# Kernel optimization log

Measured on AMD Instinct MI355X. Metric: run time of the kernel, lower is better.

The kernel has to match this reference:

```python
import jax, jax.numpy as jnp
import numpy as np

N = 2_097_152
EPS = 1e-6


def _tri(x):
    # triangleWave (period 2), maps R -> [0, 1]; applied to 'normalize=True' tables
    return 2.0 * jnp.abs(x / 2.0 - jnp.floor(x / 2.0 + 0.5))


def _grid2d(uv, table, bilinear, normalize):
    # uv: (N,2) in [0,1); table: (U,V,L)
    t = _tri(table) if normalize else table
    U, V, _ = t.shape
    u = jnp.clip(uv[:, 0], 0.0, 1.0 - EPS) * (U - 1)
    v = jnp.clip(uv[:, 1], 0.0, 1.0 - EPS) * (V - 1)
    if bilinear:
        u0 = jnp.floor(u)
        v0 = jnp.floor(v)
        fu = (u - u0)[:, None]
        fv = (v - v0)[:, None]
        u0i = u0.astype(jnp.int32)
        v0i = v0.astype(jnp.int32)
        u1i = jnp.minimum(u0i + 1, U - 1)
        v1i = jnp.minimum(v0i + 1, V - 1)
        return (t[u0i, v0i] * (1 - fu) * (1 - fv)
                + t[u1i, v0i] * fu * (1 - fv)
                + t[u0i, v1i] * (1 - fu) * fv
                + t[u1i, v1i] * fu * fv)
    return t[jnp.round(u).astype(jnp.int32), jnp.round(v).astype(jnp.int32)]


def _grid1d(u, table, bilinear, normalize):
    # u: (N,) in [0,1); table: (U,L)
    t = _tri(table) if normalize else table
    U, _ = t.shape
    uu = jnp.clip(u, 0.0, 1.0 - EPS) * (U - 1)
    if bilinear:
        u0 = jnp.floor(uu)
        fu = (uu - u0)[:, None]
        u0i = u0.astype(jnp.int32)
        u1i = jnp.minimum(u0i + 1, U - 1)
        return t[u0i] * (1 - fu) + t[u1i] * fu
    return t[jnp.round(uu).astype(jnp.int32)]


def setup_inputs() -> dict:
    key = jax.random.key(0)
    ks = jax.random.split(key, 17)
    mk = lambda i, shape: jax.random.uniform(ks[i], shape, dtype=jnp.float32)
    names = ["roughNoh", "anisoToh", "nDotLV", "tDotLV", "metalLoh",
             "subCg", "spst", "shst", "lumCs"]
    d = {n: mk(i, (N, 2)) for i, n in enumerate(names)}
    d["tabRAEnc"] = mk(9, (2048, 2048, 2))
    d["tabCgEnc"] = mk(10, (2048, 1))
    d["tabRSEnc"] = mk(11, (64, 64, 3))
    d["tabRADec"] = mk(12, (48, 48, 3))
    d["tabCgDec"] = mk(13, (96, 2))
    d["tabLVR"] = mk(14, (32, 32, 1))
    d["tabLV"] = mk(15, (32, 32, 4))
    d["tabNHL"] = mk(16, (32, 32, 4))
    return d


def reference(roughNoh, anisoToh, nDotLV, tDotLV, metalLoh, subCg, spst, shst,
              lumCs, tabRAEnc, tabCgEnc, tabRSEnc, tabRADec, tabCgDec,
              tabLVR, tabLV, tabNHL):
    raIn = jnp.stack((roughNoh[:, 0], anisoToh[:, 0]), axis=1)  # (N,2)
    metallicity = metalLoh[:, 0]
    # ---- encoder: LUT lookups + elementwise mixing coefficients ----
    ra = _grid2d(raIn, tabRAEnc, bilinear=False, normalize=True)           # (N,2)
    cg = _grid1d(subCg[:, 1], tabCgEnc, bilinear=False, normalize=True)    # (N,1)
    rsEnc = _grid2d(jnp.concatenate((raIn[:, 0:1], subCg[:, 0:1]), axis=1),
                    tabRSEnc, bilinear=True, normalize=True)               # (N,3)
    cd = (1 - metallicity) * lumCs[:, 0]
    cm0 = (spst[:, 0] * 0.1 * (1 - metallicity) * spst[:, 1]
           + metallicity * lumCs[:, 0])[:, None]
    cm1 = (spst[:, 0] * 0.1 * (1 - metallicity) * (1 - spst[:, 1]))[:, None]
    cs0 = (shst[:, 0] * (1 - metallicity) * shst[:, 1])[:, None]
    cs1 = (shst[:, 0] * (1 - metallicity) * (1 - shst[:, 1]))[:, None]
    cc = (0.25 * 0.25 * lumCs[:, 1])[:, None]
    rsCd = rsEnc * cd[:, None]                                             # (N,3)
    # ---- decoder LUTs ----
    raCoefs = _grid2d(ra, tabRADec, bilinear=True, normalize=False)        # (N,3)
    cgCoefs = _grid1d(cg[:, 0], tabCgDec, bilinear=True, normalize=False)  # (N,2)
    vTerm = _grid2d(jnp.concatenate((nDotLV[:, 0:1] * nDotLV[:, 1:2],
                                     ra[:, 0:1]), axis=1),
                    tabLVR, bilinear=True, normalize=True)                 # (N,1)
    nlvCoefs = _grid2d(nDotLV, tabLV, bilinear=True, normalize=True)       # (N,4)
    nhlCoefs = _grid2d(jnp.stack((metalLoh[:, 1], nDotLV[:, 0]), axis=1),
                       tabNHL, bilinear=True, normalize=True)              # (N,4)
    # ---- elementwise shading combination ----
    noh2 = roughNoh[:, 1] ** 2
    den = raCoefs[:, 0] * anisoToh[:, 1] ** 2 + raCoefs[:, 1] * noh2 + raCoefs[:, 2]
    dTerm = (0.25 / (nDotLV[:, 1] * den ** 2))[:, None]
    x = (rsCd[:, 0:1] * metalLoh[:, 1:2] * nlvCoefs[:, 1:2]
         + rsCd[:, 1:2] * nlvCoefs[:, 2:3]
         + rsCd[:, 2:3] * nlvCoefs[:, 3:4]
         + cm0 * vTerm * nhlCoefs[:, 2:3] * dTerm
         + cs0 * nhlCoefs[:, 0:1])
    y = (((1 - cm1) * nhlCoefs[:, 3:4] + cm1) * vTerm * dTerm
         + cs1 * nhlCoefs[:, 0:1]
         + cc * nhlCoefs[:, 1:2] * nlvCoefs[:, 0:1]
           / (nDotLV[:, 1] * (cgCoefs[:, 0] * noh2 + cgCoefs[:, 1]))[:, None])
    return jnp.concatenate((x, y), axis=1)  # (N,2)
```

## Files before the change

### kernel.cpp

```cpp
#include <hip/hip_runtime.h>
#include <hip/hip_fp16.h>

#define CLIP_HI (1.0f - 1e-6f)

typedef float f4v __attribute__((ext_vector_type(4)));

__device__ __forceinline__ float tri_(float x) {
    return 2.0f * fabsf(x * 0.5f - floorf(x * 0.5f + 0.5f));
}

__device__ __forceinline__ float clamp01(float x) {
    return fminf(fmaxf(x, 0.0f), CLIP_HI);
}

__device__ __forceinline__ float4 nt_load4(const float* p) {
    f4v v = __builtin_nontemporal_load((const f4v*)p);
    return make_float4(v.x, v.y, v.z, v.w);
}
__device__ __forceinline__ void nt_store4(float* p, float4 v) {
    f4v t = {v.x, v.y, v.z, v.w};
    __builtin_nontemporal_store(t, (f4v*)p);
}

struct H4 { __half2 xy, zw; };

struct BW {
    int i00, i10, i01, i11;
    float w00, w10, w01, w11;
};

template <int U, int V>
__device__ __forceinline__ BW bw2d(float uc, float vc) {
    float u = clamp01(uc) * (float)(U - 1);
    float v = clamp01(vc) * (float)(V - 1);
    float u0f = floorf(u), v0f = floorf(v);
    float fu = u - u0f, fv = v - v0f;
    int u0 = (int)u0f, v0 = (int)v0f;
    BW r;
    r.i00 = u0 * V + v0;
    r.i10 = r.i00 + V;
    r.i01 = r.i00 + 1;
    r.i11 = r.i10 + 1;
    float gu = 1.0f - fu, gv = 1.0f - fv;
    r.w00 = gu * gv; r.w10 = fu * gv; r.w01 = gu * fv; r.w11 = fu * fv;
    return r;
}

__device__ __forceinline__ float4 h4_blend(H4 A, H4 B, H4 C, H4 D, const BW& b) {
    float2 Axy = __half22float2(A.xy), Azw = __half22float2(A.zw);
    float2 Bxy = __half22float2(B.xy), Bzw = __half22float2(B.zw);
    float2 Cxy = __half22float2(C.xy), Czw = __half22float2(C.zw);
    float2 Dxy = __half22float2(D.xy), Dzw = __half22float2(D.zw);
    return make_float4(
        Axy.x * b.w00 + Bxy.x * b.w10 + Cxy.x * b.w01 + Dxy.x * b.w11,
        Axy.y * b.w00 + Bxy.y * b.w10 + Cxy.y * b.w01 + Dxy.y * b.w11,
        Azw.x * b.w00 + Bzw.x * b.w10 + Czw.x * b.w01 + Dzw.x * b.w11,
        Azw.y * b.w00 + Bzw.y * b.w10 + Czw.y * b.w01 + Dzw.y * b.w11);
}

__global__ __launch_bounds__(256) void prep_kernel(const float* __restrict__ t_rs,
                                                   const float* __restrict__ t_cge,
                                                   const float* __restrict__ t_cgd,
                                                   const float* __restrict__ t_rad,
                                                   H4* __restrict__ o_rs,
                                                   __half2* __restrict__ o_cg,
                                                   H4* __restrict__ o_rad) {
    int j = blockIdx.x * 256 + threadIdx.x;
    if (j < 64 * 64) {
        float a = tri_(t_rs[j * 3 + 0]);
        float b = tri_(t_rs[j * 3 + 1]);
        float c = tri_(t_rs[j * 3 + 2]);
        H4 h;
        h.xy = __floats2half2_rn(a, b);
        h.zw = __floats2half2_rn(c, 0.0f);
        o_rs[j] = h;
    }
    if (j < 2048) {
        float cg = tri_(t_cge[j]);
        float u = clamp01(cg) * 95.0f;
        float u0f = floorf(u);
        float fu = u - u0f;
        int u0 = (int)u0f;
        int u1 = min(u0 + 1, 95);
        float2 a = ((const float2*)t_cgd)[u0];
        float2 b = ((const float2*)t_cgd)[u1];
        o_cg[j] = __floats2half2_rn(a.x * (1.0f - fu) + b.x * fu,
                                    a.y * (1.0f - fu) + b.y * fu);
    }
    if (j < 48 * 48) {
        H4 h;
        h.xy = __floats2half2_rn(t_rad[j * 3 + 0], t_rad[j * 3 + 1]);
        h.zw = __floats2half2_rn(t_rad[j * 3 + 2], 0.0f);
        o_rad[j] = h;
    }
}

__device__ __forceinline__ float2 gatherRA(const float* __restrict__ tabRAEnc,
                                           float rNx, float aTx) {
    int ui = (int)rintf(clamp01(rNx) * 2047.0f);
    int vi = (int)rintf(clamp01(aTx) * 2047.0f);
    return ((const float2*)tabRAEnc)[ui * 2048 + vi];
}

template <bool USE_WS>
__device__ __forceinline__ float2 shadeB(
    float rNx, float rNy, float aTy, float nLVx, float nLVy,
    float mLx, float mLy, float sCx, float sCy, float spx, float spy,
    float shx, float shy, float lCx, float lCy,
    float2 raT,
    const float* __restrict__ tabRSEnc, const H4* __restrict__ rsPacked,
    const float* __restrict__ tabRADec, const H4* __restrict__ raDec,
    const float* __restrict__ tabCgEnc, const float* __restrict__ tabCgDec,
    const __half2* __restrict__ cgComp,
    const __half* sLVR, const H4* sLV, const H4* sNHL)
{
    float rs0, rs1, rs2;
    {
        BW b = bw2d<64, 64>(rNx, sCx);
        if constexpr (USE_WS) {
            float4 r = h4_blend(rsPacked[b.i00], rsPacked[b.i10],
                                rsPacked[b.i01], rsPacked[b.i11], b);
            rs0 = r.x; rs1 = r.y; rs2 = r.z;
        } else {
            const float* p00 = tabRSEnc + b.i00 * 3;
            const float* p10 = tabRSEnc + b.i10 * 3;
            const float* p01 = tabRSEnc + b.i01 * 3;
            const float* p11 = tabRSEnc + b.i11 * 3;
            rs0 = tri_(p00[0]) * b.w00 + tri_(p10[0]) * b.w10 + tri_(p01[0]) * b.w01 + tri_(p11[0]) * b.w11;
            rs1 = tri_(p00[1]) * b.w00 + tri_(p10[1]) * b.w10 + tri_(p01[1]) * b.w01 + tri_(p11[1]) * b.w11;
            rs2 = tri_(p00[2]) * b.w00 + tri_(p10[2]) * b.w10 + tri_(p01[2]) * b.w01 + tri_(p11[2]) * b.w11;
        }
    }

    float2 cgC;
    {
        int ci = (int)rintf(clamp01(sCy) * 2047.0f);
        if constexpr (USE_WS) {
            cgC = __half22float2(cgComp[ci]);
        } else {
            float cg = tri_(tabCgEnc[ci]);
            float u = clamp01(cg) * 95.0f;
            float u0f = floorf(u);
            float fu = u - u0f;
            int u0 = (int)u0f;
            int u1 = min(u0 + 1, 95);
            float2 a = ((const float2*)tabCgDec)[u0];
            float2 b = ((const float2*)tabCgDec)[u1];
            cgC = make_float2(a.x * (1.0f - fu) + b.x * fu,
                              a.y * (1.0f - fu) + b.y * fu);
        }
    }

    float4 nlv, nhl;
    {
        BW b = bw2d<32, 32>(nLVx, nLVy);
        nlv = h4_blend(sLV[b.i00], sLV[b.i10], sLV[b.i01], sLV[b.i11], b);
    }
    {
        BW b = bw2d<32, 32>(mLy, nLVx);
        nhl = h4_blend(sNHL[b.i00], sNHL[b.i10], sNHL[b.i01], sNHL[b.i11], b);
    }

    float ra0 = tri_(raT.x);
    float ra1 = tri_(raT.y);

    float raC0, raC1, raC2;
    {
        BW b = bw2d<48, 48>(ra0, ra1);
        if constexpr (USE_WS) {
            float4 r = h4_blend(raDec[b.i00], raDec[b.i10],
                                raDec[b.i01], raDec[b.i11], b);
            raC0 = r.x; raC1 = r.y; raC2 = r.z;
        } else {
            const float* p00 = tabRADec + b.i00 * 3;
            const float* p10 = tabRADec + b.i10 * 3;
            const float* p01 = tabRADec + b.i01 * 3;
            const float* p11 = tabRADec + b.i11 * 3;
            raC0 = p00[0] * b.w00 + p10[0] * b.w10 + p01[0] * b.w01 + p11[0] * b.w11;
            raC1 = p00[1] * b.w00 + p10[1] * b.w10 + p01[1] * b.w01 + p11[1] * b.w11;
            raC2 = p00[2] * b.w00 + p10[2] * b.w10 + p01[2] * b.w01 + p11[2] * b.w11;
        }
    }

    float vTerm;
    {
        BW b = bw2d<32, 32>(nLVx * nLVy, ra0);
        vTerm = __half2float(sLVR[b.i00]) * b.w00 + __half2float(sLVR[b.i10]) * b.w10 +
                __half2float(sLVR[b.i01]) * b.w01 + __half2float(sLVR[b.i11]) * b.w11;
    }

    float met = mLx;
    float om  = 1.0f - met;
    float cd  = om * lCx;
    float cm0 = spx * 0.1f * om * spy + met * lCx;
    float cm1 = spx * 0.1f * om * (1.0f - spy);
    float cs0 = shx * om * shy;
    float cs1 = shx * om * (1.0f - shy);
    float cc  = 0.0625f * lCy;

    float noh2 = rNy * rNy;
    float den  = raC0 * aTy * aTy + raC1 * noh2 + raC2;
    float dTerm = 0.25f / (nLVy * den * den);

    float x = rs0 * cd * mLy * nlv.y + rs1 * cd * nlv.z + rs2 * cd * nlv.w
            + cm0 * vTerm * nhl.z * dTerm + cs0 * nhl.x;

    float y = ((1.0f - cm1) * nhl.w + cm1) * vTerm * dTerm
            + cs1 * nhl.x
            + cc * nhl.y * nlv.x / (nLVy * (cgC.x * noh2 + cgC.y));

    return make_float2(x, y);
}

template <bool USE_WS>
__global__ __launch_bounds__(256, 4) void disney_main(
    const float* __restrict__ roughNoh,
    const float* __restrict__ anisoToh,
    const float* __restrict__ nDotLV,
    const float* __restrict__ metalLoh,
    const float* __restrict__ subCg,
    const float* __restrict__ spst,
    const float* __restrict__ shst,
    const float* __restrict__ lumCs,
    const float* __restrict__ tabRAEnc,
    const float* __restrict__ tabCgEnc,
    const float* __restrict__ tabCgDec,
    const float* __restrict__ tabRSEnc,
    const float* __restrict__ tabRADec,
    const H4*    __restrict__ rsPacked,
    const __half2* __restrict__ cgComp,
    const H4*    __restrict__ raDec,
    const float* __restrict__ tabLVR,
    const float* __restrict__ tabLV,
    const float* __restrict__ tabNHL,
    float* __restrict__ out,
    int n)
{
    __shared__ __half  sLVR[1024];
    __shared__ H4      sLV[1024];
    __shared__ H4      sNHL[1024];

    int tid = threadIdx.x;

#pragma unroll
    for (int k = 0; k < 4; ++k) {
        int j = tid + k * 256;
        sLVR[j] = __float2half(tri_(tabLVR[j]));
        float4 v = ((const float4*)tabLV)[j];
        H4 h; h.xy = __floats2half2_rn(tri_(v.x), tri_(v.y));
              h.zw = __floats2half2_rn(tri_(v.z), tri_(v.w));
        sLV[j] = h;
        float4 w = ((const float4*)tabNHL)[j];
        H4 h2; h2.xy = __floats2half2_rn(tri_(w.x), tri_(w.y));
               h2.zw = __floats2half2_rn(tri_(w.z), tri_(w.w));
        sNHL[j] = h2;
    }
    __syncthreads();

    int P = (n + 1) >> 1;
    int H = (P + 1) >> 1;
    int t = blockIdx.x * 256 + tid;
    if (t >= H) return;
    int p1 = t;
    int p2 = t + H;

    bool full1 = (2 * p1 + 1) < n;
    bool full2 = (p2 < P) && ((2 * p2 + 1) < n);

    if (full1 && full2) {
        float4 rN1 = nt_load4(roughNoh + 4 * p1);
        float4 aT1 = nt_load4(anisoToh + 4 * p1);
        float4 rN2 = nt_load4(roughNoh + 4 * p2);
        float4 aT2 = nt_load4(anisoToh + 4 * p2);

        float2 raT0 = gatherRA(tabRAEnc, rN1.x, aT1.x);
        float2 raT1 = gatherRA(tabRAEnc, rN1.z, aT1.z);
        float2 raT2 = gatherRA(tabRAEnc, rN2.x, aT2.x);
        float2 raT3 = gatherRA(tabRAEnc, rN2.z, aT2.z);

        float4 nLV1 = nt_load4(nDotLV   + 4 * p1);
        float4 mL1  = nt_load4(metalLoh + 4 * p1);
        float4 sC1  = nt_load4(subCg    + 4 * p1);
        float4 sp1  = nt_load4(spst     + 4 * p1);
        float4 sh1  = nt_load4(shst     + 4 * p1);
        float4 lC1  = nt_load4(lumCs    + 4 * p1);
        float4 nLV2 = nt_load4(nDotLV   + 4 * p2);
        float4 mL2  = nt_load4(metalLoh + 4 * p2);
        float4 sC2  = nt_load4(subCg    + 4 * p2);
        float4 sp2  = nt_load4(spst     + 4 * p2);
        float4 sh2  = nt_load4(shst     + 4 * p2);
        float4 lC2  = nt_load4(lumCs    + 4 * p2);

        float2 r0 = shadeB<USE_WS>(rN1.x, rN1.y, aT1.y, nLV1.x, nLV1.y,
                                   mL1.x, mL1.y, sC1.x, sC1.y, sp1.x, sp1.y,
                                   sh1.x, sh1.y, lC1.x, lC1.y, raT0,
                                   tabRSEnc, rsPacked, tabRADec, raDec,
                                   tabCgEnc, tabCgDec, cgComp,
                                   sLVR, sLV, sNHL);
        float2 r1 = shadeB<USE_WS>(rN1.z, rN1.w, aT1.w, nLV1.z, nLV1.w,
                                   mL1.z, mL1.w, sC1.z, sC1.w, sp1.z, sp1.w,
                                   sh1.z, sh1.w, lC1.z, lC1.w, raT1,
                                   tabRSEnc, rsPacked, tabRADec, raDec,
                                   tabCgEnc, tabCgDec, cgComp,
                                   sLVR, sLV, sNHL);
        nt_store4(out + 4 * p1, make_float4(r0.x, r0.y, r1.x, r1.y));

        float2 r2 = shadeB<USE_WS>(rN2.x, rN2.y, aT2.y, nLV2.x, nLV2.y,
                                   mL2.x, mL2.y, sC2.x, sC2.y, sp2.x, sp2.y,
                                   sh2.x, sh2.y, lC2.x, lC2.y, raT2,
                                   tabRSEnc, rsPacked, tabRADec, raDec,
                                   tabCgEnc, tabCgDec, cgComp,
                                   sLVR, sLV, sNHL);
        float2 r3 = shadeB<USE_WS>(rN2.z, rN2.w, aT2.w, nLV2.z, nLV2.w,
                                   mL2.z, mL2.w, sC2.z, sC2.w, sp2.z, sp2.w,
                                   sh2.z, sh2.w, lC2.z, lC2.w, raT3,
                                   tabRSEnc, rsPacked, tabRADec, raDec,
                                   tabCgEnc, tabCgDec, cgComp,
                                   sLVR, sLV, sNHL);
        nt_store4(out + 4 * p2, make_float4(r2.x, r2.y, r3.x, r3.y));
    } else {
        int es[4] = { 2 * p1, 2 * p1 + 1,
                      (p2 < P) ? 2 * p2 : n, (p2 < P) ? 2 * p2 + 1 : n };
#pragma unroll
        for (int k = 0; k < 4; ++k) {
            int e = es[k];
            if (e >= n) continue;
            float2 rN  = ((const float2*)roughNoh)[e];
            float2 aT  = ((const float2*)anisoToh)[e];
            float2 nLV = ((const float2*)nDotLV)[e];
            float2 mL  = ((const float2*)metalLoh)[e];
            float2 sC  = ((const float2*)subCg)[e];
            float2 sp  = ((const float2*)spst)[e];
            float2 sh  = ((const float2*)shst)[e];
            float2 lC  = ((const float2*)lumCs)[e];
            float2 raT = gatherRA(tabRAEnc, rN.x, aT.x);
            float2 r = shadeB<USE_WS>(rN.x, rN.y, aT.y, nLV.x, nLV.y,
                                      mL.x, mL.y, sC.x, sC.y, sp.x, sp.y,
                                      sh.x, sh.y, lC.x, lC.y, raT,
                                      tabRSEnc, rsPacked, tabRADec, raDec,
                                      tabCgEnc, tabCgDec, cgComp,
                                      sLVR, sLV, sNHL);
            ((float2*)out)[e] = r;
        }
    }
}

extern "C" void kernel_launch(void* const* d_in, const int* in_sizes, int n_in,
                              void* d_out, int out_size, void* d_ws, size_t ws_size,
                              hipStream_t stream) {
    const float* roughNoh = (const float*)d_in[0];
    const float* anisoToh = (const float*)d_in[1];
    const float* nDotLV   = (const float*)d_in[2];
    const float* metalLoh = (const float*)d_in[4];
    const float* subCg    = (const float*)d_in[5];
    const float* spst     = (const float*)d_in[6];
    const float* shst     = (const float*)d_in[7];
    const float* lumCs    = (const float*)d_in[8];
    const float* tabRAEnc = (const float*)d_in[9];
    const float* tabCgEnc = (const float*)d_in[10];
    const float* tabRSEnc = (const float*)d_in[11];
    const float* tabRADec = (const float*)d_in[12];
    const float* tabCgDec = (const float*)d_in[13];
    const float* tabLVR   = (const float*)d_in[14];
    const float* tabLV    = (const float*)d_in[15];
    const float* tabNHL   = (const float*)d_in[16];

    int n = in_sizes[0] / 2;
    float* out = (float*)d_out;

    const int block = 256;
    int P = (n + 1) / 2;
    int H = (P + 1) / 2;
    int grid = (H + block - 1) / block;

    const size_t OFF_CG  = 64 * 64 * sizeof(H4);
    const size_t OFF_RAD = OFF_CG + 2048 * sizeof(__half2);
    const size_t WS_NEED = OFF_RAD + 48 * 48 * sizeof(H4);
    bool use_ws = ws_size >= WS_NEED;
    H4*      ws_rs  = (H4*)d_ws;
    __half2* ws_cg  = (__half2*)((char*)d_ws + OFF_CG);
    H4*      ws_rad = (H4*)((char*)d_ws + OFF_RAD);

    if (use_ws) {
        prep_kernel<<<(64 * 64 + 255) / 256, 256, 0, stream>>>(
            tabRSEnc, tabCgEnc, tabCgDec, tabRADec, ws_rs, ws_cg, ws_rad);
        disney_main<true><<<grid, block, 0, stream>>>(
            roughNoh, anisoToh, nDotLV, metalLoh, subCg, spst, shst, lumCs,
            tabRAEnc, tabCgEnc, tabCgDec, tabRSEnc, tabRADec,
            ws_rs, ws_cg, ws_rad,
            tabLVR, tabLV, tabNHL, out, n);
    } else {
        disney_main<false><<<grid, block, 0, stream>>>(
            roughNoh, anisoToh, nDotLV, metalLoh, subCg, spst, shst, lumCs,
            tabRAEnc, tabCgEnc, tabCgDec, tabRSEnc, tabRADec,
            ws_rs, ws_cg, ws_rad,
            tabLVR, tabLV, tabNHL, out, n);
    }
}
```

Measured before the change: 244.9 us.

## Stage RS and RA-decode tables in LDS with split half2/half layout

Moves the 64x64 RS table and the 48x48 RA-decode table into shared memory as packed half2 plus half arrays, replacing global gathers with LDS lookups. The block size is doubled to 512 so the per-block table-loading cost is spread over more pixels. The RA-decode prep pass now happens inside each block. This adds about 38KB of LDS per block, which may limit occupancy, and the table fill is repeated in every block.

```diff
diff --git a/kernel.cpp b/kernel.cpp
--- a/kernel.cpp
+++ b/kernel.cpp
@@ -58,22 +58,33 @@
         Azw.y * b.w00 + Bzw.y * b.w10 + Czw.y * b.w01 + Dzw.y * b.w11);
 }
 
+__device__ __forceinline__ float3 blend3(const __half2* tAB, const __half* tC,
+                                         const BW& b) {
+    float2 A = __half22float2(tAB[b.i00]);
+    float2 B = __half22float2(tAB[b.i10]);
+    float2 C = __half22float2(tAB[b.i01]);
+    float2 D = __half22float2(tAB[b.i11]);
+    float3 r;
+    r.x = A.x * b.w00 + B.x * b.w10 + C.x * b.w01 + D.x * b.w11;
+    r.y = A.y * b.w00 + B.y * b.w10 + C.y * b.w01 + D.y * b.w11;
+    r.z = __half2float(tC[b.i00]) * b.w00 + __half2float(tC[b.i10]) * b.w10 +
+          __half2float(tC[b.i01]) * b.w01 + __half2float(tC[b.i11]) * b.w11;
+    return r;
+}
+
 __global__ __launch_bounds__(256) void prep_kernel(const float* __restrict__ t_rs,
                                                    const float* __restrict__ t_cge,
                                                    const float* __restrict__ t_cgd,
-                                                   const float* __restrict__ t_rad,
-                                                   H4* __restrict__ o_rs,
-                                                   __half2* __restrict__ o_cg,
-                                                   H4* __restrict__ o_rad) {
+                                                   __half2* __restrict__ o_rsAB,
+                                                   __half* __restrict__ o_rsC,
+                                                   __half2* __restrict__ o_cg) {
     int j = blockIdx.x * 256 + threadIdx.x;
     if (j < 64 * 64) {
         float a = tri_(t_rs[j * 3 + 0]);
         float b = tri_(t_rs[j * 3 + 1]);
         float c = tri_(t_rs[j * 3 + 2]);
-        H4 h;
-        h.xy = __floats2half2_rn(a, b);
-        h.zw = __floats2half2_rn(c, 0.0f);
-        o_rs[j] = h;
+        o_rsAB[j] = __floats2half2_rn(a, b);
+        o_rsC[j]  = __float2half(c);
     }
     if (j < 2048) {
         float cg = tri_(t_cge[j]);
@@ -87,12 +98,6 @@
         o_cg[j] = __floats2half2_rn(a.x * (1.0f - fu) + b.x * fu,
                                     a.y * (1.0f - fu) + b.y * fu);
     }
-    if (j < 48 * 48) {
-        H4 h;
-        h.xy = __floats2half2_rn(t_rad[j * 3 + 0], t_rad[j * 3 + 1]);
-        h.zw = __floats2half2_rn(t_rad[j * 3 + 2], 0.0f);
-        o_rad[j] = h;
-    }
 }
 
 __device__ __forceinline__ float2 gatherRA(const float* __restrict__ tabRAEnc,
@@ -108,28 +113,17 @@
     float mLx, float mLy, float sCx, float sCy, float spx, float spy,
     float shx, float shy, float lCx, float lCy,
     float2 raT,
-    const float* __restrict__ tabRSEnc, const H4* __restrict__ rsPacked,
-    const float* __restrict__ tabRADec, const H4* __restrict__ raDec,
+    const __half2* __restrict__ cgComp,
     const float* __restrict__ tabCgEnc, const float* __restrict__ tabCgDec,
-    const __half2* __restrict__ cgComp,
+    const __half2* sRsAB, const __half* sRsC,
+    const __half2* sRadAB, const __half* sRadC,
     const __half* sLVR, const H4* sLV, const H4* sNHL)
 {
     float rs0, rs1, rs2;
     {
         BW b = bw2d<64, 64>(rNx, sCx);
-        if constexpr (USE_WS) {
-            float4 r = h4_blend(rsPacked[b.i00], rsPacked[b.i10],
-                                rsPacked[b.i01], rsPacked[b.i11], b);
-            rs0 = r.x; rs1 = r.y; rs2 = r.z;
-        } else {
-            const float* p00 = tabRSEnc + b.i00 * 3;
-            const float* p10 = tabRSEnc + b.i10 * 3;
-            const float* p01 = tabRSEnc + b.i01 * 3;
-            const float* p11 = tabRSEnc + b.i11 * 3;
-            rs0 = tri_(p00[0]) * b.w00 + tri_(p10[0]) * b.w10 + tri_(p01[0]) * b.w01 + tri_(p11[0]) * b.w11;
-            rs1 = tri_(p00[1]) * b.w00 + tri_(p10[1]) * b.w10 + tri_(p01[1]) * b.w01 + tri_(p11[1]) * b.w11;
-            rs2 = tri_(p00[2]) * b.w00 + tri_(p10[2]) * b.w10 + tri_(p01[2]) * b.w01 + tri_(p11[2]) * b.w11;
-        }
+        float3 r = blend3(sRsAB, sRsC, b);
+        rs0 = r.x; rs1 = r.y; rs2 = r.z;
     }
 
     float2 cgC;
@@ -167,19 +161,8 @@
     float raC0, raC1, raC2;
     {
         BW b = bw2d<48, 48>(ra0, ra1);
-        if constexpr (USE_WS) {
-            float4 r = h4_blend(raDec[b.i00], raDec[b.i10],
-                                raDec[b.i01], raDec[b.i11], b);
-            raC0 = r.x; raC1 = r.y; raC2 = r.z;
-        } else {
-            const float* p00 = tabRADec + b.i00 * 3;
-            const float* p10 = tabRADec + b.i10 * 3;
-            const float* p01 = tabRADec + b.i01 * 3;
-            const float* p11 = tabRADec + b.i11 * 3;
-            raC0 = p00[0] * b.w00 + p10[0] * b.w10 + p01[0] * b.w01 + p11[0] * b.w11;
-            raC1 = p00[1] * b.w00 + p10[1] * b.w10 + p01[1] * b.w01 + p11[1] * b.w11;
-            raC2 = p00[2] * b.w00 + p10[2] * b.w10 + p01[2] * b.w01 + p11[2] * b.w11;
-        }
+        float3 r = blend3(sRadAB, sRadC, b);
+        raC0 = r.x; raC1 = r.y; raC2 = r.z;
     }
 
     float vTerm;
@@ -213,7 +196,7 @@
 }
 
 template <bool USE_WS>
-__global__ __launch_bounds__(256, 4) void disney_main(
+__global__ __launch_bounds__(512, 4) void disney_main(
     const float* __restrict__ roughNoh,
     const float* __restrict__ anisoToh,
     const float* __restrict__ nDotLV,
@@ -227,24 +210,46 @@
     const float* __restrict__ tabCgDec,
     const float* __restrict__ tabRSEnc,
     const float* __restrict__ tabRADec,
-    const H4*    __restrict__ rsPacked,
+    const __half2* __restrict__ wsRsAB,
+    const __half*  __restrict__ wsRsC,
     const __half2* __restrict__ cgComp,
-    const H4*    __restrict__ raDec,
     const float* __restrict__ tabLVR,
     const float* __restrict__ tabLV,
     const float* __restrict__ tabNHL,
     float* __restrict__ out,
     int n)
 {
+    __shared__ __half2 sRsAB[4096];
+    __shared__ __half  sRsC [4096];
+    __shared__ __half2 sRadAB[2304];
+    __shared__ __half  sRadC [2304];
     __shared__ __half  sLVR[1024];
-    __shared__ H4      sLV[1024];
+    __shared__ H4      sLV [1024];
     __shared__ H4      sNHL[1024];
 
     int tid = threadIdx.x;
 
 #pragma unroll
-    for (int k = 0; k < 4; ++k) {
-        int j = tid + k * 256;
+    for (int k = 0; k < 8; ++k) {
+        int j = tid + k * 512;
+        if constexpr (USE_WS) {
+            sRsAB[j] = wsRsAB[j];
+            sRsC[j]  = wsRsC[j];
+        } else {
+            float a = tri_(tabRSEnc[j * 3 + 0]);
+            float b = tri_(tabRSEnc[j * 3 + 1]);
+            float c = tri_(tabRSEnc[j * 3 + 2]);
+            sRsAB[j] = __floats2half2_rn(a, b);
+            sRsC[j]  = __float2half(c);
+        }
+    }
+    for (int j = tid; j < 2304; j += 512) {
+        sRadAB[j] = __floats2half2_rn(tabRADec[j * 3 + 0], tabRADec[j * 3 + 1]);
+        sRadC[j]  = __float2half(tabRADec[j * 3 + 2]);
+    }
+#pragma unroll
+    for (int k = 0; k < 2; ++k) {
+        int j = tid + k * 512;
         sLVR[j] = __float2half(tri_(tabLVR[j]));
         float4 v = ((const float4*)tabLV)[j];
         H4 h; h.xy = __floats2half2_rn(tri_(v.x), tri_(v.y));
@@ -259,7 +264,7 @@
 
     int P = (n + 1) >> 1;
     int H = (P + 1) >> 1;
-    int t = blockIdx.x * 256 + tid;
+    int t = blockIdx.x * 512 + tid;
     if (t >= H) return;
     int p1 = t;
     int p2 = t + H;
@@ -294,28 +299,28 @@
         float2 r0 = shadeB<USE_WS>(rN1.x, rN1.y, aT1.y, nLV1.x, nLV1.y,
                                    mL1.x, mL1.y, sC1.x, sC1.y, sp1.x, sp1.y,
                                    sh1.x, sh1.y, lC1.x, lC1.y, raT0,
-                                   tabRSEnc, rsPacked, tabRADec, raDec,
-                                   tabCgEnc, tabCgDec, cgComp,
+                                   cgComp, tabCgEnc, tabCgDec,
+                                   sRsAB, sRsC, sRadAB, sRadC,
                                    sLVR, sLV, sNHL);
         float2 r1 = shadeB<USE_WS>(rN1.z, rN1.w, aT1.w, nLV1.z, nLV1.w,
                                    mL1.z, mL1.w, sC1.z, sC1.w, sp1.z, sp1.w,
                                    sh1.z, sh1.w, lC1.z, lC1.w, raT1,
-                                   tabRSEnc, rsPacked, tabRADec, raDec,
-                                   tabCgEnc, tabCgDec, cgComp,
+                                   cgComp, tabCgEnc, tabCgDec,
+                                   sRsAB, sRsC, sRadAB, sRadC,
                                    sLVR, sLV, sNHL);
         nt_store4(out + 4 * p1, make_float4(r0.x, r0.y, r1.x, r1.y));
 
         float2 r2 = shadeB<USE_WS>(rN2.x, rN2.y, aT2.y, nLV2.x, nLV2.y,
                                    mL2.x, mL2.y, sC2.x, sC2.y, sp2.x, sp2.y,
                                    sh2.x, sh2.y, lC2.x, lC2.y, raT2,
-                                   tabRSEnc, rsPacked, tabRADec, raDec,
-                                   tabCgEnc, tabCgDec, cgComp,
+                                   cgComp, tabCgEnc, tabCgDec,
+                                   sRsAB, sRsC, sRadAB, sRadC,
                                    sLVR, sLV, sNHL);
         float2 r3 = shadeB<USE_WS>(rN2.z, rN2.w, aT2.w, nLV2.z, nLV2.w,
                                    mL2.z, mL2.w, sC2.z, sC2.w, sp2.z, sp2.w,
                                    sh2.z, sh2.w, lC2.z, lC2.w, raT3,
-                                   tabRSEnc, rsPacked, tabRADec, raDec,
-                                   tabCgEnc, tabCgDec, cgComp,
+                                   cgComp, tabCgEnc, tabCgDec,
+                                   sRsAB, sRsC, sRadAB, sRadC,
                                    sLVR, sLV, sNHL);
         nt_store4(out + 4 * p2, make_float4(r2.x, r2.y, r3.x, r3.y));
     } else {
@@ -337,8 +342,8 @@
             float2 r = shadeB<USE_WS>(rN.x, rN.y, aT.y, nLV.x, nLV.y,
                                       mL.x, mL.y, sC.x, sC.y, sp.x, sp.y,
                                       sh.x, sh.y, lC.x, lC.y, raT,
-                                      tabRSEnc, rsPacked, tabRADec, raDec,
-                                      tabCgEnc, tabCgDec, cgComp,
+                                      cgComp, tabCgEnc, tabCgDec,
+                                      sRsAB, sRsC, sRadAB, sRadC,
                                       sLVR, sLV, sNHL);
             ((float2*)out)[e] = r;
         }
@@ -368,32 +373,32 @@
     int n = in_sizes[0] / 2;
     float* out = (float*)d_out;
 
-    const int block = 256;
+    const int block = 512;
     int P = (n + 1) / 2;
     int H = (P + 1) / 2;
     int grid = (H + block - 1) / block;
 
-    const size_t OFF_CG  = 64 * 64 * sizeof(H4);
-    const size_t OFF_RAD = OFF_CG + 2048 * sizeof(__half2);
-    const size_t WS_NEED = OFF_RAD + 48 * 48 * sizeof(H4);
+    const size_t OFF_RSC = 4096 * sizeof(__half2);
+    const size_t OFF_CG  = OFF_RSC + 4096 * sizeof(__half);
+    const size_t WS_NEED = OFF_CG + 2048 * sizeof(__half2);
     bool use_ws = ws_size >= WS_NEED;
-    H4*      ws_rs  = (H4*)d_ws;
-    __half2* ws_cg  = (__half2*)((char*)d_ws + OFF_CG);
-    H4*      ws_rad = (H4*)((char*)d_ws + OFF_RAD);
+    __half2* ws_rsAB = (__half2*)d_ws;
+    __half*  ws_rsC  = (__half*)((char*)d_ws + OFF_RSC);
+    __half2* ws_cg   = (__half2*)((char*)d_ws + OFF_CG);
 
     if (use_ws) {
         prep_kernel<<<(64 * 64 + 255) / 256, 256, 0, stream>>>(
-            tabRSEnc, tabCgEnc, tabCgDec, tabRADec, ws_rs, ws_cg, ws_rad);
+            tabRSEnc, tabCgEnc, tabCgDec, ws_rsAB, ws_rsC, ws_cg);
         disney_main<true><<<grid, block, 0, stream>>>(
             roughNoh, anisoToh, nDotLV, metalLoh, subCg, spst, shst, lumCs,
             tabRAEnc, tabCgEnc, tabCgDec, tabRSEnc, tabRADec,
-            ws_rs, ws_cg, ws_rad,
+            ws_rsAB, ws_rsC, ws_cg,
             tabLVR, tabLV, tabNHL, out, n);
     } else {
         disney_main<false><<<grid, block, 0, stream>>>(
             roughNoh, anisoToh, nDotLV, metalLoh, subCg, spst, shst, lumCs,
             tabRAEnc, tabCgEnc, tabCgDec, tabRSEnc, tabRADec,
-            ws_rs, ws_cg, ws_rad,
+            ws_rsAB, ws_rsC, ws_cg,
             tabLVR, tabLV, tabNHL, out, n);
     }
 }
```

Result: faster. 227.1 us (-7.3%).
